# Optimization experiments

Hardware: AMD Instinct MI355X
Metric: run time of the kernel (lower is better)

Reference implementation:

```python
import jax, jax.numpy as jnp
import numpy as np

TOP_K = 2


def setup_inputs() -> dict:
    key = jax.random.key(0)
    k1, k2 = jax.random.split(key)
    x = jax.random.normal(k1, (4, 4096, 2048), dtype=jnp.float32)
    W = jax.random.normal(k2, (64, 2048), dtype=jnp.float32) * (1.0 / np.sqrt(2048))
    return {"x": x, "W": W}


def reference(x, W):
    B, S, D = x.shape
    E = W.shape[0]
    # logits: [B*S, E] via linear router (no bias)
    flat = x.reshape(-1, D)
    logits = jnp.einsum('td,ed->te', flat, W)
    probs = jax.nn.softmax(logits, axis=-1)
    # eval path: top-k indices
    _, top_k_indices = jax.lax.top_k(probs, TOP_K)          # [T, K]
    # scatter 1s -> mask; scatter gathered probs -> router_probs (== probs*mask)
    router_mask = jax.nn.one_hot(top_k_indices, E, dtype=probs.dtype).sum(axis=-2)  # [T, E]
    router_probs = probs * router_mask
    # normalize (top_k > 1: gradient flows through the sum)
    router_probs = router_probs / router_probs.sum(axis=-1, keepdims=True)
    return (router_mask.reshape(B, S, E),
            top_k_indices.reshape(B, S, TOP_K),
            router_probs.reshape(B, S, E),
            probs.reshape(B, S, E))
```

## Files before the change

### kernel.cpp

```cpp
#include <hip/hip_runtime.h>
#include <math.h>


#define D_DIM 2048
#define E_DIM 64
#define TM 64
#define KB 64
#define NCH (D_DIM / KB)
#define LDST 72

typedef __bf16 bf16x8 __attribute__((ext_vector_type(8)));
typedef float f32x4 __attribute__((ext_vector_type(4)));

static __device__ __forceinline__ unsigned short f2bf(float f) {
    unsigned int u = __float_as_uint(f);
    u += 0x7fffu + ((u >> 16) & 1u);
    return (unsigned short)(u >> 16);
}
static __device__ __forceinline__ float bf2f(unsigned short h) {
    return __uint_as_float(((unsigned int)h) << 16);
}
static __device__ __forceinline__ void split4(const float4 v, ushort4* h, ushort4* l) {
    h->x = f2bf(v.x); l->x = f2bf(v.x - bf2f(h->x));
    h->y = f2bf(v.y); l->y = f2bf(v.y - bf2f(h->y));
    h->z = f2bf(v.z); l->z = f2bf(v.z - bf2f(h->z));
    h->w = f2bf(v.w); l->w = f2bf(v.w - bf2f(h->w));
}

__global__ __launch_bounds__(256, 1) void router_fused(
    const float* __restrict__ x, const float* __restrict__ W,
    float* __restrict__ mask_out, float* __restrict__ idx_out,
    float* __restrict__ rp_out, float* __restrict__ probs_out)
{
    __shared__ __align__(16) unsigned short XH[TM * LDST];
    __shared__ __align__(16) unsigned short XL[TM * LDST];
    __shared__ __align__(16) unsigned short WH[E_DIM * LDST];
    __shared__ __align__(16) unsigned short WL[E_DIM * LDST];
    __shared__ float LG[TM * 65];

    const int tid  = threadIdx.x;
    const int lane = tid & 63;
    const int wv   = tid >> 6;
    const int quad = lane >> 4;
    const int l16  = lane & 15;
    const int t0   = blockIdx.x * TM;

    const float4* x4 = (const float4*)x;
    const float4* w4 = (const float4*)W;

    const int r0 = tid >> 4;
    const int c4 = tid & 15;

    f32x4 acc[4];
    #pragma unroll
    for (int n = 0; n < 4; ++n) { f32x4 z = {0.f, 0.f, 0.f, 0.f}; acc[n] = z; }

    float4 xr[4], wr[4];
    #pragma unroll
    for (int i = 0; i < 4; ++i) {
        int row = r0 + 16 * i;
        xr[i] = x4[(t0 + row) * 512 + c4];
        wr[i] = w4[row * 512 + c4];
    }

    for (int ch = 0; ch < NCH; ++ch) {
        #pragma unroll
        for (int i = 0; i < 4; ++i) {
            int row = r0 + 16 * i;
            ushort4 h, l;
            split4(xr[i], &h, &l);
            *(ushort4*)&XH[row * LDST + c4 * 4] = h;
            *(ushort4*)&XL[row * LDST + c4 * 4] = l;
            split4(wr[i], &h, &l);
            *(ushort4*)&WH[row * LDST + c4 * 4] = h;
            *(ushort4*)&WL[row * LDST + c4 * 4] = l;
        }
        __syncthreads();

        if (ch + 1 < NCH) {
            #pragma unroll
            for (int i = 0; i < 4; ++i) {
                int row = r0 + 16 * i;
                xr[i] = x4[(t0 + row) * 512 + (ch + 1) * 16 + c4];
                wr[i] = w4[row * 512 + (ch + 1) * 16 + c4];
            }
        }

        #pragma unroll
        for (int ks = 0; ks < 2; ++ks) {
            const int kofs = ks * 32 + quad * 8;
            bf16x8 ah = *(const bf16x8*)&XH[(16 * wv + l16) * LDST + kofs];
            bf16x8 al = *(const bf16x8*)&XL[(16 * wv + l16) * LDST + kofs];
            #pragma unroll
            for (int n = 0; n < 4; ++n) {
                bf16x8 bh = *(const bf16x8*)&WH[(16 * n + l16) * LDST + kofs];
                bf16x8 bl = *(const bf16x8*)&WL[(16 * n + l16) * LDST + kofs];
                acc[n] = __builtin_amdgcn_mfma_f32_16x16x32_bf16(ah, bh, acc[n], 0, 0, 0);
                acc[n] = __builtin_amdgcn_mfma_f32_16x16x32_bf16(al, bh, acc[n], 0, 0, 0);
                acc[n] = __builtin_amdgcn_mfma_f32_16x16x32_bf16(ah, bl, acc[n], 0, 0, 0);
            }
        }
        __syncthreads();
    }

    #pragma unroll
    for (int n = 0; n < 4; ++n) {
        #pragma unroll
        for (int r = 0; r < 4; ++r) {
            int tl = 16 * wv + quad * 4 + r;
            int e  = 16 * n + l16;
            LG[tl * 65 + e] = acc[n][r];
        }
    }

    for (int i = 0; i < 16; ++i) {
        int tl = 16 * wv + i;
        float v = LG[tl * 65 + lane];

        float bv = v; int bi = lane;
        #pragma unroll
        for (int off = 1; off < 64; off <<= 1) {
            float ov = __shfl_xor(bv, off, 64);
            int   oi = __shfl_xor(bi, off, 64);
            bool take = (ov > bv) || (ov == bv && oi < bi);
            bv = take ? ov : bv;
            bi = take ? oi : bi;
        }
        float m = bv; int i1 = bi;

        float p = __expf(v - m);
        float s = p;
        #pragma unroll
        for (int off = 1; off < 64; off <<= 1) s += __shfl_xor(s, off, 64);
        float prob = p / s;

        float v2 = (lane == i1) ? -INFINITY : v;
        float bv2 = v2; int bi2 = lane;
        #pragma unroll
        for (int off = 1; off < 64; off <<= 1) {
            float ov = __shfl_xor(bv2, off, 64);
            int   oi = __shfl_xor(bi2, off, 64);
            bool take = (ov > bv2) || (ov == bv2 && oi < bi2);
            bv2 = take ? ov : bv2;
            bi2 = take ? oi : bi2;
        }
        int i2 = bi2;

        float pd = __shfl(prob, i1, 64) + __shfl(prob, i2, 64);
        int t = t0 + tl;
        bool top = (lane == i1) || (lane == i2);

        mask_out[t * 64 + lane]  = top ? 1.f : 0.f;
        rp_out[t * 64 + lane]    = top ? prob / pd : 0.f;
        probs_out[t * 64 + lane] = prob;
        if (lane == 0) {
            idx_out[t * 2]     = (float)i1;
            idx_out[t * 2 + 1] = (float)i2;
        }
    }
}

extern "C" void kernel_launch(void* const* d_in, const int* in_sizes, int n_in,
                              void* d_out, int out_size, void* d_ws, size_t ws_size,
                              hipStream_t stream) {
    const float* x = (const float*)d_in[0];
    const float* W = (const float*)d_in[1];
    float* out = (float*)d_out;

    const int T = in_sizes[0] / D_DIM;
    float* mask_out  = out;
    float* idx_out   = out + (size_t)T * E_DIM;
    float* rp_out    = idx_out + (size_t)T * 2;
    float* probs_out = rp_out + (size_t)T * E_DIM;

    router_fused<<<dim3(T / TM), dim3(256), 0, stream>>>(
        x, W, mask_out, idx_out, rp_out, probs_out);
}
```

Measured before the change: 228.9 us.

## Split K across waves, pre-split W to bf16 once, load operands directly from global

```diff
diff --git a/kernel.cpp b/kernel.cpp
--- a/kernel.cpp
+++ b/kernel.cpp
@@ -4,12 +4,12 @@
 
 #define D_DIM 2048
 #define E_DIM 64
-#define TM 64
-#define KB 64
-#define NCH (D_DIM / KB)
-#define LDST 72
+#define TPB 16
+#define KSPLIT 4
+#define KSTEPS 16
 
 typedef __bf16 bf16x8 __attribute__((ext_vector_type(8)));
+typedef unsigned short us8 __attribute__((ext_vector_type(8)));
 typedef float f32x4 __attribute__((ext_vector_type(4)));
 
 static __device__ __forceinline__ unsigned short f2bf(float f) {
@@ -27,94 +27,88 @@
     h->w = f2bf(v.w); l->w = f2bf(v.w - bf2f(h->w));
 }
 
-__global__ __launch_bounds__(256, 1) void router_fused(
-    const float* __restrict__ x, const float* __restrict__ W,
+__global__ __launch_bounds__(256, 1) void convert_w(
+    const float4* __restrict__ W4, unsigned short* __restrict__ WH,
+    unsigned short* __restrict__ WL)
+{
+    int i = blockIdx.x * 256 + threadIdx.x;
+    float4 v = W4[i];
+    ushort4 h, l;
+    split4(v, &h, &l);
+    *(ushort4*)&WH[i * 4] = h;
+    *(ushort4*)&WL[i * 4] = l;
+}
+
+__global__ __launch_bounds__(256, 4) void router_fused(
+    const float* __restrict__ x,
+    const unsigned short* __restrict__ WH, const unsigned short* __restrict__ WL,
     float* __restrict__ mask_out, float* __restrict__ idx_out,
     float* __restrict__ rp_out, float* __restrict__ probs_out)
 {
-    __shared__ __align__(16) unsigned short XH[TM * LDST];
-    __shared__ __align__(16) unsigned short XL[TM * LDST];
-    __shared__ __align__(16) unsigned short WH[E_DIM * LDST];
-    __shared__ __align__(16) unsigned short WL[E_DIM * LDST];
-    __shared__ float LG[TM * 65];
+    __shared__ float PART[KSPLIT * 64 * 16];
+    __shared__ float LG[TPB * 65];
 
     const int tid  = threadIdx.x;
     const int lane = tid & 63;
     const int wv   = tid >> 6;
     const int quad = lane >> 4;
     const int l16  = lane & 15;
-    const int t0   = blockIdx.x * TM;
+    const int t0   = blockIdx.x * TPB;
 
     const float4* x4 = (const float4*)x;
-    const float4* w4 = (const float4*)W;
-
-    const int r0 = tid >> 4;
-    const int c4 = tid & 15;
+    const size_t xbase = (size_t)(t0 + l16) * 512 + wv * 128 + quad * 2;
+    const int wbase = l16 * 2048 + wv * 512 + quad * 8;
 
     f32x4 acc[4];
     #pragma unroll
     for (int n = 0; n < 4; ++n) { f32x4 z = {0.f, 0.f, 0.f, 0.f}; acc[n] = z; }
 
-    float4 xr[4], wr[4];
-    #pragma unroll
-    for (int i = 0; i < 4; ++i) {
-        int row = r0 + 16 * i;
-        xr[i] = x4[(t0 + row) * 512 + c4];
-        wr[i] = w4[row * 512 + c4];
-    }
+    float4 xa = x4[xbase];
+    float4 xb = x4[xbase + 1];
 
-    for (int ch = 0; ch < NCH; ++ch) {
-        #pragma unroll
-        for (int i = 0; i < 4; ++i) {
-            int row = r0 + 16 * i;
-            ushort4 h, l;
-            split4(xr[i], &h, &l);
-            *(ushort4*)&XH[row * LDST + c4 * 4] = h;
-            *(ushort4*)&XL[row * LDST + c4 * 4] = l;
-            split4(wr[i], &h, &l);
-            *(ushort4*)&WH[row * LDST + c4 * 4] = h;
-            *(ushort4*)&WL[row * LDST + c4 * 4] = l;
-        }
-        __syncthreads();
+    for (int ks = 0; ks < KSTEPS; ++ks) {
+        ushort4 h0, l0, h1, l1;
+        split4(xa, &h0, &l0);
+        split4(xb, &h1, &l1);
+        union { us8 u; bf16x8 b; } ua, ul;
+        ua.u = (us8){h0.x, h0.y, h0.z, h0.w, h1.x, h1.y, h1.z, h1.w};
+        ul.u = (us8){l0.x, l0.y, l0.z, l0.w, l1.x, l1.y, l1.z, l1.w};
+        bf16x8 ah = ua.b, al = ul.b;
 
-        if (ch + 1 < NCH) {
-            #pragma unroll
-            for (int i = 0; i < 4; ++i) {
-                int row = r0 + 16 * i;
-                xr[i] = x4[(t0 + row) * 512 + (ch + 1) * 16 + c4];
-                wr[i] = w4[row * 512 + (ch + 1) * 16 + c4];
-            }
+        if (ks + 1 < KSTEPS) {
+            xa = x4[xbase + (ks + 1) * 8];
+            xb = x4[xbase + (ks + 1) * 8 + 1];
         }
 
+        const int ko = ks * 32;
         #pragma unroll
-        for (int ks = 0; ks < 2; ++ks) {
-            const int kofs = ks * 32 + quad * 8;
-            bf16x8 ah = *(const bf16x8*)&XH[(16 * wv + l16) * LDST + kofs];
-            bf16x8 al = *(const bf16x8*)&XL[(16 * wv + l16) * LDST + kofs];
-            #pragma unroll
-            for (int n = 0; n < 4; ++n) {
-                bf16x8 bh = *(const bf16x8*)&WH[(16 * n + l16) * LDST + kofs];
-                bf16x8 bl = *(const bf16x8*)&WL[(16 * n + l16) * LDST + kofs];
-                acc[n] = __builtin_amdgcn_mfma_f32_16x16x32_bf16(ah, bh, acc[n], 0, 0, 0);
-                acc[n] = __builtin_amdgcn_mfma_f32_16x16x32_bf16(al, bh, acc[n], 0, 0, 0);
-                acc[n] = __builtin_amdgcn_mfma_f32_16x16x32_bf16(ah, bl, acc[n], 0, 0, 0);
-            }
+        for (int n = 0; n < 4; ++n) {
+            bf16x8 bh = *(const bf16x8*)(WH + wbase + n * 32768 + ko);
+            bf16x8 bl = *(const bf16x8*)(WL + wbase + n * 32768 + ko);
+            acc[n] = __builtin_amdgcn_mfma_f32_16x16x32_bf16(ah, bh, acc[n], 0, 0, 0);
+            acc[n] = __builtin_amdgcn_mfma_f32_16x16x32_bf16(al, bh, acc[n], 0, 0, 0);
+            acc[n] = __builtin_amdgcn_mfma_f32_16x16x32_bf16(ah, bl, acc[n], 0, 0, 0);
         }
-        __syncthreads();
     }
 
     #pragma unroll
-    for (int n = 0; n < 4; ++n) {
+    for (int n = 0; n < 4; ++n)
         #pragma unroll
-        for (int r = 0; r < 4; ++r) {
-            int tl = 16 * wv + quad * 4 + r;
-            int e  = 16 * n + l16;
-            LG[tl * 65 + e] = acc[n][r];
-        }
+        for (int r = 0; r < 4; ++r)
+            PART[wv * 1024 + lane * 16 + n * 4 + r] = acc[n][r];
+    __syncthreads();
+
+    #pragma unroll
+    for (int c = 0; c < 4; ++c) {
+        int idx = tid * 4 + c;
+        int t = idx >> 6, e = idx & 63;
+        int off = ((t >> 2) * 16 + (e & 15)) * 16 + ((e >> 4) * 4 + (t & 3));
+        LG[t * 65 + e] = PART[off] + PART[1024 + off] + PART[2048 + off] + PART[3072 + off];
     }
+    __syncthreads();
 
-    for (int i = 0; i < 16; ++i) {
-        int tl = 16 * wv + i;
+    for (int i = 0; i < 4; ++i) {
+        int tl = wv * 4 + i;
         float v = LG[tl * 65 + lane];
 
         float bv = v; int bi = lane;
@@ -168,11 +162,17 @@
     float* out = (float*)d_out;
 
     const int T = in_sizes[0] / D_DIM;
+    const int WN = in_sizes[1];
+
+    unsigned short* WH = (unsigned short*)d_ws;
+    unsigned short* WL = WH + WN;
+
     float* mask_out  = out;
     float* idx_out   = out + (size_t)T * E_DIM;
     float* rp_out    = idx_out + (size_t)T * 2;
     float* probs_out = rp_out + (size_t)T * E_DIM;
 
-    router_fused<<<dim3(T / TM), dim3(256), 0, stream>>>(
-        x, W, mask_out, idx_out, rp_out, probs_out);
+    convert_w<<<dim3(WN / 4 / 256), dim3(256), 0, stream>>>((const float4*)W, WH, WL);
+    router_fused<<<dim3(T / TPB), dim3(256), 0, stream>>>(
+        x, WH, WL, mask_out, idx_out, rp_out, probs_out);
 }
```

After: 253.3 us. 1.11x slower.
